# Performance work log

Hardware: AMD Instinct MI355X
Metric: run time of the kernel (lower is better)

The kernel has to match this reference:

```python
import jax, jax.numpy as jnp
import numpy as np

B, N, IN_DIM, DIM, KNN = 8, 2048, 128, 128, 16
POS_H = 64
ATTN_H = DIM * 4
EPS = 1e-5
SCALE = 1.0 / np.sqrt(DIM).astype(np.float32)


def setup_inputs() -> dict:
    key = jax.random.key(0)
    ks = jax.random.split(key, 10)
    nrm = lambda k, shape, s=0.02: jax.random.normal(k, shape, jnp.float32) * s
    return dict(
        ori_x=jax.random.normal(ks[0], (B, N, IN_DIM), jnp.float32),
        pos=jax.random.normal(ks[1], (B, N, 3), jnp.float32),
        w_in=nrm(ks[2], (IN_DIM, DIM)),
        w_qkv=nrm(ks[3], (DIM, 3 * DIM)),
        w_out=nrm(ks[4], (DIM, IN_DIM)),
        pos_w1=nrm(ks[5], (3, POS_H)), pos_b1=jnp.zeros((POS_H,), jnp.float32),
        pos_bn_g=jnp.ones((POS_H,), jnp.float32), pos_bn_b=jnp.zeros((POS_H,), jnp.float32),
        pos_bn_m=jnp.zeros((POS_H,), jnp.float32), pos_bn_v=jnp.ones((POS_H,), jnp.float32),
        pos_w2=nrm(ks[6], (POS_H, DIM)), pos_b2=jnp.zeros((DIM,), jnp.float32),
        attn_w1=nrm(ks[7], (DIM, ATTN_H)), attn_b1=jnp.zeros((ATTN_H,), jnp.float32),
        attn_bn_g=jnp.ones((ATTN_H,), jnp.float32), attn_bn_b=jnp.zeros((ATTN_H,), jnp.float32),
        attn_bn_m=jnp.zeros((ATTN_H,), jnp.float32), attn_bn_v=jnp.ones((ATTN_H,), jnp.float32),
        attn_w2=nrm(ks[8], (ATTN_H, DIM)), attn_b2=jnp.zeros((DIM,), jnp.float32),
    )


def _bn_eval(x, g, b, m, v):
    # BatchNorm2d in eval mode; channel is the last axis in our [b,n,k,C] layout
    return (x - m) * (g * jax.lax.rsqrt(v + EPS)) + b


def reference(ori_x, pos, w_in, w_qkv, w_out,
              pos_w1, pos_b1, pos_bn_g, pos_bn_b, pos_bn_m, pos_bn_v, pos_w2, pos_b2,
              attn_w1, attn_b1, attn_bn_g, attn_bn_b, attn_bn_m, attn_bn_v, attn_w2, attn_b2):
    x = ori_x @ w_in                                  # [b,n,dim]
    qkv = x @ w_qkv
    q, k, v = jnp.split(qkv, 3, axis=-1)              # each [b,n,dim]

    # pairwise squared distances [b,n,n] (monotone in rel_dist -> same topk)
    sq = jnp.sum(pos * pos, axis=-1)
    d2 = sq[:, :, None] + sq[:, None, :] - 2.0 * jnp.einsum('bnd,bmd->bnm', pos, pos)
    _, idx = jax.lax.top_k(-d2, KNN)                  # [b,n,KNN] nearest neighbors

    gather = jax.vmap(lambda t, i: t[i])              # [n,C],[n,k] -> [n,k,C] per batch
    k_g = gather(k, idx)                              # [b,n,k,dim]
    v_g = gather(v, idx)
    pos_g = gather(pos, idx)                          # [b,n,k,3]

    rel_pos = pos[:, :, None, :] - pos_g              # [b,n,k,3]
    pe = jax.nn.relu(_bn_eval(rel_pos @ pos_w1 + pos_b1, pos_bn_g, pos_bn_b, pos_bn_m, pos_bn_v))
    pe = pe @ pos_w2 + pos_b2                         # [b,n,k,dim]

    qk_rel = q[:, :, None, :] - k_g                   # [b,n,k,dim]
    h = jax.nn.relu(_bn_eval((qk_rel + pe) @ attn_w1 + attn_b1,
                             attn_bn_g, attn_bn_b, attn_bn_m, attn_bn_v))
    h = h @ attn_w2 + attn_b2                         # [b,n,k,dim]

    attn = jax.nn.softmax(h * SCALE, axis=-2)         # softmax over neighbors
    agg = jnp.sum(attn * (v_g + pe), axis=2)          # [b,n,dim]
    return agg @ w_out + ori_x
```

## Files before the change

kernel.cpp:

```cpp
#include <hip/hip_runtime.h>

#define EPS 1e-5f

constexpr int NB   = 8;
constexpr int NN   = 2048;
constexpr int DIM  = 128;
constexpr int KNN  = 16;
constexpr int AH   = 512;
constexpr int NPTS = NB * NN;
constexpr float SCALE = 0.08838834764831845f;

typedef __attribute__((ext_vector_type(8))) short short8;
typedef __attribute__((ext_vector_type(4))) float floatx4;

__device__ __forceinline__ short f2bf(float f) {
  union { float f; unsigned u; } a; a.f = f;
  return (short)((a.u + 0x8000u) >> 16);
}
__device__ __forceinline__ float bf2f(short s) {
  union { unsigned u; float f; } a; a.u = ((unsigned)(unsigned short)s) << 16;
  return a.f;
}

__global__ __launch_bounds__(256) void pack_weights(
    const float* __restrict__ attn_w1, const float* __restrict__ attn_w2,
    const float* __restrict__ pos_w2, const float* __restrict__ w_in,
    const float* __restrict__ w_qkv,
    const float* __restrict__ w_out, const float* __restrict__ pos,
    const float* __restrict__ attn_b1, const float* __restrict__ abn_g,
    const float* __restrict__ abn_b, const float* __restrict__ abn_m,
    const float* __restrict__ abn_v,
    const float* __restrict__ pos_b1, const float* __restrict__ pbn_g,
    const float* __restrict__ pbn_b, const float* __restrict__ pbn_m,
    const float* __restrict__ pbn_v, const float* __restrict__ pos_b2,
    short* __restrict__ w1p, short* __restrict__ w2p, short* __restrict__ pw2p,
    short* __restrict__ wfp, short* __restrict__ wop,
    float* __restrict__ biasq,
    float* __restrict__ t1sc, float* __restrict__ t1bi,
    float* __restrict__ phsc, float* __restrict__ phbi,
    float* __restrict__ pos_t)
{
  int t = blockIdx.x * 256 + threadIdx.x;
  if (t < 65536) {
    int k = t >> 9, n = t & 511;
    int ks = k >> 5, q = (k >> 3) & 3, j = k & 7;
    int ch = n >> 6, nt = (n >> 4) & 3, cc = n & 15;
    int dst = ch * 8192 + nt * 2048 + ks * 512 + (q * 16 + cc) * 8 + j;
    w1p[dst] = f2bf(attn_w1[t]);
  } else if (t < 131072) {
    int s = t - 65536;
    int k = s >> 7, n = s & 127;
    int ch = k >> 6, r = k & 63;
    int ks = r >> 5, q = (r >> 3) & 3, j = r & 7;
    int nt = n >> 4, cc = n & 15;
    int dst = ch * 8192 + nt * 1024 + ks * 512 + (q * 16 + cc) * 8 + j;
    w2p[dst] = f2bf(attn_w2[s]);
  } else if (t < 139264) {
    int s = t - 131072;
    int k = s >> 7, n = s & 127;
    int ks = k >> 5, r = k & 31, q = r >> 3, j = r & 7;
    int nt = n >> 4, cc = n & 15;
    int dst = nt * 1024 + ks * 512 + (q * 16 + cc) * 8 + j;
    pw2p[dst] = f2bf(pos_w2[s]);
  } else if (t < 188416) {
    int e = t - 139264;
    int j = e & 7, lane = (e >> 3) & 63, ks = (e >> 9) & 3, nt = (e >> 11) & 7, nc = e >> 14;
    int q = lane >> 4, cc = lane & 15;
    int k = ks * 32 + q * 8 + j, n = nc * 128 + nt * 16 + cc;
    float s = 0.0f;
#pragma unroll 8
    for (int m = 0; m < 128; ++m)
      s += w_in[(size_t)k * DIM + m] * w_qkv[(size_t)m * 384 + n];
    wfp[e] = f2bf(s);
  } else if (t < 204800) {
    int s = t - 188416;
    int k = s >> 7, n = s & 127;
    int ks = k >> 5, q = (k >> 3) & 3, j = k & 7;
    int nt = n >> 4, cc = n & 15;
    int dst = nt * 2048 + ks * 512 + (q * 16 + cc) * 8 + j;
    wop[dst] = f2bf(w_out[s]);
  } else if (t < 205184) {
    int c = t - 204800;
    biasq[c] = (c < 128) ? pos_b2[c] : ((c < 256) ? 0.0f : pos_b2[c - 256]);
  } else if (t < 205696) {
    int c = t - 205184;
    t1sc[c] = abn_g[c] * rsqrtf(abn_v[c] + EPS);
  } else if (t < 206208) {
    int c = t - 205696;
    float sc = abn_g[c] * rsqrtf(abn_v[c] + EPS);
    t1bi[c] = (attn_b1[c] - abn_m[c]) * sc + abn_b[c];
  } else if (t < 206272) {
    int c = t - 206208;
    phsc[c] = pbn_g[c] * rsqrtf(pbn_v[c] + EPS);
  } else if (t < 206336) {
    int c = t - 206272;
    float sc = pbn_g[c] * rsqrtf(pbn_v[c] + EPS);
    phbi[c] = (pos_b1[c] - pbn_m[c]) * sc + pbn_b[c];
  } else if (t < 206336 + NPTS * 3) {
    int e = t - 206336;
    int p = e / 3, d = e - p * 3;
    int b = p >> 11, n = p & (NN - 1);
    pos_t[((size_t)b * 3 + d) * NN + n] = pos[e];
  }
}

__global__ __launch_bounds__(256, 4) void knn_gemm_in(
    const float* __restrict__ A, const short* __restrict__ wfp,
    const float* __restrict__ biasq, short* __restrict__ C,
    const float* __restrict__ pos_t, int* __restrict__ idx_out)
{
  __shared__ short As[64 * 128];
  const int tid = threadIdx.x;
  const int bx = blockIdx.x;

  if (bx % 9 == 0) {
    const int lane = tid & 63, w = tid >> 6;
    const int wr = w >> 1, wc = w & 1;
    const int q = lane >> 4, cc = lane & 15;
    const int row0 = (bx / 9) * 64;
#pragma unroll
    for (int it = 0; it < 4; ++it) {
      int e = tid + it * 256;
      int row = e >> 4, cg = e & 15;
      const float* src = A + (size_t)(row0 + row) * 128 + cg * 8;
      float4 f0 = *(const float4*)src, f1 = *(const float4*)(src + 4);
      short8 v;
      v[0] = f2bf(f0.x); v[1] = f2bf(f0.y); v[2] = f2bf(f0.z); v[3] = f2bf(f0.w);
      v[4] = f2bf(f1.x); v[5] = f2bf(f1.y); v[6] = f2bf(f1.z); v[7] = f2bf(f1.w);
      *(short8*)(As + row * 128 + ((cg ^ (row & 15)) << 3)) = v;
    }
    __syncthreads();
    for (int nc = 0; nc < 3; ++nc) {
      floatx4 acc[2][4];
#pragma unroll
      for (int i = 0; i < 2; ++i)
#pragma unroll
        for (int jt = 0; jt < 4; ++jt) acc[i][jt] = (floatx4){0.f, 0.f, 0.f, 0.f};
#pragma unroll
      for (int ks = 0; ks < 4; ++ks) {
        short8 a8[2], b8[4];
#pragma unroll
        for (int i = 0; i < 2; ++i) {
          int row = (wr * 2 + i) * 16 + cc;
          a8[i] = *(const short8*)(As + row * 128 + (((ks * 4 + q) ^ cc) << 3));
        }
#pragma unroll
        for (int jt = 0; jt < 4; ++jt)
          b8[jt] = *(const short8*)(wfp + ((((nc * 8 + wc * 4 + jt) * 4 + ks) * 64 + lane) << 3));
#pragma unroll
        for (int i = 0; i < 2; ++i)
#pragma unroll
          for (int jt = 0; jt < 4; ++jt)
            acc[i][jt] = __builtin_amdgcn_mfma_f32_16x16x32_bf16(a8[i], b8[jt], acc[i][jt], 0, 0, 0);
      }
#pragma unroll
      for (int jt = 0; jt < 4; ++jt) {
        int colG = nc * 128 + (wc * 4 + jt) * 16 + cc;
        float bv = biasq[colG];
#pragma unroll
        for (int i = 0; i < 2; ++i)
#pragma unroll
          for (int r = 0; r < 4; ++r) {
            int row = (wr * 2 + i) * 16 + q * 4 + r;
            C[(size_t)(row0 + row) * 384 + colG] = f2bf(acc[i][jt][r] + bv);
          }
      }
    }
  } else {
    const int kb = bx - bx / 9 - 1;
    const int lane = tid & 63;
    const int p0 = kb * 8 + (tid >> 6) * 2;
    const int b = p0 >> 11, i0 = p0 & (NN - 1), i1 = i0 + 1;
    const float* px = pos_t + (size_t)b * 3 * NN;
    const float* py = px + NN;
    const float* pz = py + NN;
    const float xa = px[i0], ya = py[i0], za = pz[i0];
    const float sqa = xa * xa + ya * ya + za * za;
    const float xb = px[i1], yb = py[i1], zb = pz[i1];
    const float sqb = xb * xb + yb * yb + zb * zb;
    float va[32], vb[32];
#pragma unroll
    for (int t = 0; t < 32; ++t) {
      int j = t * 64 + lane;
      float xj = px[j], yj = py[j], zj = pz[j];
      float sqj = xj * xj + yj * yj + zj * zj;
      va[t] = sqa + sqj - 2.0f * (xa * xj + ya * yj + za * zj);
      vb[t] = sqb + sqj - 2.0f * (xb * xj + yb * yj + zb * zj);
    }
    for (int s = 0; s < KNN; ++s) {
      float av = 3.4e38f; int aj = 1 << 30;
      float bv = 3.4e38f; int bj = 1 << 30;
#pragma unroll
      for (int t = 0; t < 32; ++t) {
        if (va[t] < av) { av = va[t]; aj = t * 64 + lane; }
        if (vb[t] < bv) { bv = vb[t]; bj = t * 64 + lane; }
      }
#pragma unroll
      for (int m = 1; m < 64; m <<= 1) {
        float oav = __shfl_xor(av, m); int oaj = __shfl_xor(aj, m);
        float obv = __shfl_xor(bv, m); int obj = __shfl_xor(bj, m);
        if (oav < av || (oav == av && oaj < aj)) { av = oav; aj = oaj; }
        if (obv < bv || (obv == bv && obj < bj)) { bv = obv; bj = obj; }
      }
      if (lane == 0) {
        idx_out[(size_t)p0 * KNN + s] = aj;
        idx_out[(size_t)(p0 + 1) * KNN + s] = bj;
      }
#pragma unroll
      for (int t = 0; t < 32; ++t) {
        if (aj == t * 64 + lane) va[t] = 3.4e38f;
        if (bj == t * 64 + lane) vb[t] = 3.4e38f;
      }
    }
  }
}

__global__ __launch_bounds__(256, 3) void fused_attn(
    const float* __restrict__ pos_t, const short* __restrict__ qkv,
    const int* __restrict__ knn_idx,
    const float* __restrict__ pos_w1,
    const short* __restrict__ w1p, const short* __restrict__ w2p,
    const short* __restrict__ pw2p, const short* __restrict__ wop,
    const float* __restrict__ t1sc, const float* __restrict__ t1bi,
    const float* __restrict__ phsc, const float* __restrict__ phbi,
    const float* __restrict__ attn_b2,
    const float* __restrict__ ori_x, float* __restrict__ out)
{
  __shared__ short a_s[64 * 128];
  __shared__ short vpe_s[64 * 128];
  __shared__ short t1_s[2][64 * 64];
  __shared__ short q_ss[4 * 128];
  __shared__ float relp_s[64 * 4];
  __shared__ int   nbr_s[64];

  const int tid = threadIdx.x;
  const int lane = tid & 63, w = tid >> 6;
  const int wr = w >> 1, wc = w & 1;
  const int q = lane >> 4, cc = lane & 15;
  const int bb = blockIdx.x & 7;
  const int base = (blockIdx.x >> 3) * 4;
  const int gp0 = bb * NN + base;

  const float* px = pos_t + (size_t)bb * 3 * NN;
  const float* py = px + NN;
  const float* pz = py + NN;

  if (tid < 64) nbr_s[tid] = knn_idx[(size_t)gp0 * KNN + tid];
  else if (tid < 128) {
    int e = tid - 64;
    int p = e >> 4, seg = e & 15;
    *(short8*)(q_ss + p * 128 + seg * 8) =
        *(const short8*)(qkv + (size_t)(gp0 + p) * 384 + seg * 8);
  }
  __syncthreads();
  if (tid < 64) {
    int p = tid >> 4;
    int j = nbr_s[tid];
    relp_s[tid * 4 + 0] = px[base + p] - px[j];
    relp_s[tid * 4 + 1] = py[base + p] - py[j];
    relp_s[tid * 4 + 2] = pz[base + p] - pz[j];
  }
  __syncthreads();

#pragma unroll
  for (int r2 = 0; r2 < 16; ++r2) {
    int e = tid + r2 * 256;
    int row = e >> 6, c = e & 63;
    float lin = relp_s[row * 4] * pos_w1[c] + relp_s[row * 4 + 1] * pos_w1[64 + c]
              + relp_s[row * 4 + 2] * pos_w1[128 + c];
    t1_s[0][row * 64 + (((c >> 3) ^ (row & 7)) << 3) + (c & 7)] =
        f2bf(fmaxf(lin * phsc[c] + phbi[c], 0.0f));
  }
  __syncthreads();

  floatx4 pe[2][4];
#pragma unroll
  for (int i = 0; i < 2; ++i)
#pragma unroll
    for (int jt = 0; jt < 4; ++jt) pe[i][jt] = (floatx4){0.f, 0.f, 0.f, 0.f};
#pragma unroll
  for (int ks = 0; ks < 2; ++ks) {
    short8 a8[2];
#pragma unroll
    for (int i = 0; i < 2; ++i) {
      int row = (wr * 2 + i) * 16 + cc;
      a8[i] = *(const short8*)(t1_s[0] + row * 64 + (((ks * 4 + q) ^ (row & 7)) << 3));
    }
#pragma unroll
    for (int jt = 0; jt < 4; ++jt) {
      short8 b8 = *(const short8*)(pw2p + ((((wc * 4 + jt) * 2 + ks) * 64 + lane) << 3));
#pragma unroll
      for (int i = 0; i < 2; ++i)
        pe[i][jt] = __builtin_amdgcn_mfma_f32_16x16x32_bf16(a8[i], b8, pe[i][jt], 0, 0, 0);
    }
  }

#pragma unroll
  for (int it = 0; it < 4; ++it) {
    int e = tid + it * 256;
    int row = e >> 4, g = e & 15;
    const short* kvrow = qkv + ((size_t)bb * NN + nbr_s[row]) * 384;
    int dst = row * 128 + ((g ^ (row & 15)) << 3);
    *(short8*)(a_s + dst)   = *(const short8*)(kvrow + 128 + g * 8);
    *(short8*)(vpe_s + dst) = *(const short8*)(kvrow + 256 + g * 8);
  }
  __syncthreads();

#pragma unroll
  for (int i = 0; i < 2; ++i) {
    int rt = wr * 2 + i;
#pragma unroll
    for (int jt = 0; jt < 4; ++jt) {
      int col = (wc * 4 + jt) * 16 + cc;
      float qv = bf2f(q_ss[rt * 128 + col]);
#pragma unroll
      for (int r = 0; r < 4; ++r) {
        int row = rt * 16 + q * 4 + r;
        float pev = pe[i][jt][r];
        int slot = row * 128 + (((col >> 3) ^ (row & 15)) << 3) + (col & 7);
        a_s[slot]   = f2bf(qv - bf2f(a_s[slot]) + pev);
        vpe_s[slot] = f2bf(bf2f(vpe_s[slot]) + pev);
      }
    }
  }
  __syncthreads();

  floatx4 hacc[2][4];
#pragma unroll
  for (int i = 0; i < 2; ++i)
#pragma unroll
    for (int jt = 0; jt < 4; ++jt) hacc[i][jt] = (floatx4){0.f, 0.f, 0.f, 0.f};

  for (int ch = 0; ch < 8; ++ch) {
    short* t1b = t1_s[ch & 1];
    floatx4 tacc[2][2];
#pragma unroll
    for (int i = 0; i < 2; ++i)
#pragma unroll
      for (int jt = 0; jt < 2; ++jt) tacc[i][jt] = (floatx4){0.f, 0.f, 0.f, 0.f};
#pragma unroll
    for (int ks = 0; ks < 4; ++ks) {
      short8 a8[2], b8[2];
#pragma unroll
      for (int i = 0; i < 2; ++i) {
        int row = (wr * 2 + i) * 16 + cc;
        a8[i] = *(const short8*)(a_s + row * 128 + (((ks * 4 + q) ^ cc) << 3));
      }
#pragma unroll
      for (int jt = 0; jt < 2; ++jt)
        b8[jt] = *(const short8*)(w1p + ((((ch * 4 + wc * 2 + jt) * 4 + ks) * 64 + lane) << 3));
#pragma unroll
      for (int i = 0; i < 2; ++i)
#pragma unroll
        for (int jt = 0; jt < 2; ++jt)
          tacc[i][jt] = __builtin_amdgcn_mfma_f32_16x16x32_bf16(a8[i], b8[jt], tacc[i][jt], 0, 0, 0);
    }
#pragma unroll
    for (int jt = 0; jt < 2; ++jt) {
      int colL = (wc * 2 + jt) * 16 + cc;
      int colG = ch * 64 + colL;
      float sc = t1sc[colG], bi = t1bi[colG];
#pragma unroll
      for (int i = 0; i < 2; ++i)
#pragma unroll
        for (int r = 0; r < 4; ++r) {
          int row = (wr * 2 + i) * 16 + q * 4 + r;
          t1b[row * 64 + (((colL >> 3) ^ (row & 7)) << 3) + (colL & 7)] =
              f2bf(fmaxf(tacc[i][jt][r] * sc + bi, 0.0f));
        }
    }
    __syncthreads();
#pragma unroll
    for (int ks = 0; ks < 2; ++ks) {
      short8 a8[2], b8[4];
#pragma unroll
      for (int i = 0; i < 2; ++i) {
        int row = (wr * 2 + i) * 16 + cc;
        a8[i] = *(const short8*)(t1b + row * 64 + (((ks * 4 + q) ^ (row & 7)) << 3));
      }
#pragma unroll
      for (int jt = 0; jt < 4; ++jt)
        b8[jt] = *(const short8*)(w2p + ((((ch * 8 + wc * 4 + jt) * 2 + ks) * 64 + lane) << 3));
#pragma unroll
      for (int i = 0; i < 2; ++i)
#pragma unroll
        for (int jt = 0; jt < 4; ++jt)
          hacc[i][jt] = __builtin_amdgcn_mfma_f32_16x16x32_bf16(a8[i], b8[jt], hacc[i][jt], 0, 0, 0);
    }
  }

  short* agg_s = t1_s[0];
#pragma unroll
  for (int i = 0; i < 2; ++i) {
    int rt = wr * 2 + i;
#pragma unroll
    for (int jt = 0; jt < 4; ++jt) {
      int col = (wc * 4 + jt) * 16 + cc;
      float b2v = attn_b2[col];
      float v0[4], mx = -3.4e38f;
#pragma unroll
      for (int r = 0; r < 4; ++r) {
        v0[r] = (hacc[i][jt][r] + b2v) * SCALE;
        mx = fmaxf(mx, v0[r]);
      }
      mx = fmaxf(mx, __shfl_xor(mx, 16));
      mx = fmaxf(mx, __shfl_xor(mx, 32));
      float ex[4], sum = 0.f;
#pragma unroll
      for (int r = 0; r < 4; ++r) { ex[r] = __expf(v0[r] - mx); sum += ex[r]; }
      sum += __shfl_xor(sum, 16);
      sum += __shfl_xor(sum, 32);
      float inv = 1.0f / sum;
      float part = 0.f;
#pragma unroll
      for (int r = 0; r < 4; ++r) {
        int row = rt * 16 + q * 4 + r;
        int slot = row * 128 + (((col >> 3) ^ (row & 15)) << 3) + (col & 7);
        part += ex[r] * bf2f(vpe_s[slot]);
      }
      part += __shfl_xor(part, 16);
      part += __shfl_xor(part, 32);
      if (q == 0) agg_s[rt * 136 + col] = f2bf(part * inv);
    }
  }
  __syncthreads();

  {
    floatx4 oacc[2];
#pragma unroll
    for (int jt = 0; jt < 2; ++jt) oacc[jt] = (floatx4){0.f, 0.f, 0.f, 0.f};
#pragma unroll
    for (int ks = 0; ks < 4; ++ks) {
      short8 a8 = *(const short8*)(agg_s + cc * 136 + ks * 32 + q * 8);
#pragma unroll
      for (int jt = 0; jt < 2; ++jt) {
        short8 b8 = *(const short8*)(wop + ((((w * 2 + jt) * 4 + ks) * 64 + lane) << 3));
        oacc[jt] = __builtin_amdgcn_mfma_f32_16x16x32_bf16(a8, b8, oacc[jt], 0, 0, 0);
      }
    }
    if (q == 0) {
#pragma unroll
      for (int jt = 0; jt < 2; ++jt) {
        int col = (w * 2 + jt) * 16 + cc;
#pragma unroll
        for (int r = 0; r < 4; ++r) {
          size_t o = (size_t)(gp0 + r) * 128 + col;
          out[o] = oacc[jt][r] + ori_x[o];
        }
      }
    }
  }
}

extern "C" void kernel_launch(void* const* d_in, const int* in_sizes, int n_in,
                              void* d_out, int out_size, void* d_ws, size_t ws_size,
                              hipStream_t stream)
{
  const float* ori_x    = (const float*)d_in[0];
  const float* pos      = (const float*)d_in[1];
  const float* w_in     = (const float*)d_in[2];
  const float* w_qkv    = (const float*)d_in[3];
  const float* w_out    = (const float*)d_in[4];
  const float* pos_w1   = (const float*)d_in[5];
  const float* pos_b1   = (const float*)d_in[6];
  const float* pos_bn_g = (const float*)d_in[7];
  const float* pos_bn_b = (const float*)d_in[8];
  const float* pos_bn_m = (const float*)d_in[9];
  const float* pos_bn_v = (const float*)d_in[10];
  const float* pos_w2   = (const float*)d_in[11];
  const float* pos_b2   = (const float*)d_in[12];
  const float* attn_w1  = (const float*)d_in[13];
  const float* attn_b1  = (const float*)d_in[14];
  const float* attn_bn_g = (const float*)d_in[15];
  const float* attn_bn_b = (const float*)d_in[16];
  const float* attn_bn_m = (const float*)d_in[17];
  const float* attn_bn_v = (const float*)d_in[18];
  const float* attn_w2  = (const float*)d_in[19];
  const float* attn_b2  = (const float*)d_in[20];
  float* out = (float*)d_out;

  short* qkvb = (short*)d_ws;
  short* w1p  = qkvb + (size_t)NPTS * 3 * DIM;
  short* w2p  = w1p + 65536;
  short* pw2p = w2p + 65536;
  short* wfp  = pw2p + 8192;
  short* wop  = wfp + 49152;
  float* biasq = (float*)(wop + 16384);
  float* t1sc = biasq + 384;
  float* t1bi = t1sc + 512;
  float* phsc = t1bi + 512;
  float* phbi = phsc + 64;
  float* pos_t = phbi + 64;
  int*   idx  = (int*)(pos_t + (size_t)NB * 3 * NN);

  pack_weights<<<998, 256, 0, stream>>>(attn_w1, attn_w2, pos_w2, w_in, w_qkv,
      w_out, pos,
      attn_b1, attn_bn_g, attn_bn_b, attn_bn_m, attn_bn_v,
      pos_b1, pos_bn_g, pos_bn_b, pos_bn_m, pos_bn_v, pos_b2,
      w1p, w2p, pw2p, wfp, wop, biasq, t1sc, t1bi, phsc, phbi, pos_t);
  knn_gemm_in<<<2304, 256, 0, stream>>>(ori_x, wfp, biasq, qkvb, pos_t, idx);
  fused_attn<<<NPTS / 4, 256, 0, stream>>>(pos_t, qkvb, idx, pos_w1,
      w1p, w2p, pw2p, wop, t1sc, t1bi, phsc, phbi, attn_b2, ori_x, out);
}
```

Before: 361.9 us.

## Fold BN scales into weights and shrink fused_attn LDS for higher occupancy

Folds the batch-norm scale factors of both MLPs into the packed first-layer weights (attn_w1 and pos_w1), so the epilogues only add a bias. fused_attn's shared memory is cut by dropping the double-buffered t1 tile, the q/neighbor/relpos staging buffers and two of the three prologue barriers. Neighbor indices and q values are now read straight from global memory, and launch bounds are raised to 4 blocks per SM. The single t1 buffer needs an extra barrier in every chunk iteration, and the higher occupancy target may push registers to spill.

```diff
diff --git a/kernel.cpp b/kernel.cpp
--- a/kernel.cpp
+++ b/kernel.cpp
@@ -27,6 +27,7 @@
     const float* __restrict__ pos_w2, const float* __restrict__ w_in,
     const float* __restrict__ w_qkv,
     const float* __restrict__ w_out, const float* __restrict__ pos,
+    const float* __restrict__ pos_w1,
     const float* __restrict__ attn_b1, const float* __restrict__ abn_g,
     const float* __restrict__ abn_b, const float* __restrict__ abn_m,
     const float* __restrict__ abn_v,
@@ -35,9 +36,8 @@
     const float* __restrict__ pbn_v, const float* __restrict__ pos_b2,
     short* __restrict__ w1p, short* __restrict__ w2p, short* __restrict__ pw2p,
     short* __restrict__ wfp, short* __restrict__ wop,
-    float* __restrict__ biasq,
-    float* __restrict__ t1sc, float* __restrict__ t1bi,
-    float* __restrict__ phsc, float* __restrict__ phbi,
+    float* __restrict__ biasq, float* __restrict__ t1bi,
+    float* __restrict__ phbi, float* __restrict__ w1s,
     float* __restrict__ pos_t)
 {
   int t = blockIdx.x * 256 + threadIdx.x;
@@ -46,7 +46,8 @@
     int ks = k >> 5, q = (k >> 3) & 3, j = k & 7;
     int ch = n >> 6, nt = (n >> 4) & 3, cc = n & 15;
     int dst = ch * 8192 + nt * 2048 + ks * 512 + (q * 16 + cc) * 8 + j;
-    w1p[dst] = f2bf(attn_w1[t]);
+    float sc = abn_g[n] * rsqrtf(abn_v[n] + EPS);
+    w1p[dst] = f2bf(attn_w1[t] * sc);
   } else if (t < 131072) {
     int s = t - 65536;
     int k = s >> 7, n = s & 127;
@@ -84,20 +85,19 @@
     biasq[c] = (c < 128) ? pos_b2[c] : ((c < 256) ? 0.0f : pos_b2[c - 256]);
   } else if (t < 205696) {
     int c = t - 205184;
-    t1sc[c] = abn_g[c] * rsqrtf(abn_v[c] + EPS);
-  } else if (t < 206208) {
-    int c = t - 205696;
     float sc = abn_g[c] * rsqrtf(abn_v[c] + EPS);
     t1bi[c] = (attn_b1[c] - abn_m[c]) * sc + abn_b[c];
-  } else if (t < 206272) {
-    int c = t - 206208;
-    phsc[c] = pbn_g[c] * rsqrtf(pbn_v[c] + EPS);
-  } else if (t < 206336) {
-    int c = t - 206272;
+  } else if (t < 205760) {
+    int c = t - 205696;
     float sc = pbn_g[c] * rsqrtf(pbn_v[c] + EPS);
     phbi[c] = (pos_b1[c] - pbn_m[c]) * sc + pbn_b[c];
-  } else if (t < 206336 + NPTS * 3) {
-    int e = t - 206336;
+  } else if (t < 205952) {
+    int e = t - 205760;
+    int c = e & 63;
+    float sc = pbn_g[c] * rsqrtf(pbn_v[c] + EPS);
+    w1s[e] = pos_w1[e] * sc;
+  } else if (t < 205952 + NPTS * 3) {
+    int e = t - 205952;
     int p = e / 3, d = e - p * 3;
     int b = p >> 11, n = p & (NN - 1);
     pos_t[((size_t)b * 3 + d) * NN + n] = pos[e];
@@ -215,23 +215,19 @@
   }
 }
 
-__global__ __launch_bounds__(256, 3) void fused_attn(
+__global__ __launch_bounds__(256, 4) void fused_attn(
     const float* __restrict__ pos_t, const short* __restrict__ qkv,
     const int* __restrict__ knn_idx,
-    const float* __restrict__ pos_w1,
+    const float* __restrict__ w1s,
     const short* __restrict__ w1p, const short* __restrict__ w2p,
     const short* __restrict__ pw2p, const short* __restrict__ wop,
-    const float* __restrict__ t1sc, const float* __restrict__ t1bi,
-    const float* __restrict__ phsc, const float* __restrict__ phbi,
+    const float* __restrict__ t1bi, const float* __restrict__ phbi,
     const float* __restrict__ attn_b2,
     const float* __restrict__ ori_x, float* __restrict__ out)
 {
   __shared__ short a_s[64 * 128];
   __shared__ short vpe_s[64 * 128];
-  __shared__ short t1_s[2][64 * 64];
-  __shared__ short q_ss[4 * 128];
-  __shared__ float relp_s[64 * 4];
-  __shared__ int   nbr_s[64];
+  __shared__ short t1_s[64 * 64];
 
   const int tid = threadIdx.x;
   const int lane = tid & 63, w = tid >> 6;
@@ -245,74 +241,65 @@
   const float* py = px + NN;
   const float* pz = py + NN;
 
-  if (tid < 64) nbr_s[tid] = knn_idx[(size_t)gp0 * KNN + tid];
-  else if (tid < 128) {
-    int e = tid - 64;
-    int p = e >> 4, seg = e & 15;
-    *(short8*)(q_ss + p * 128 + seg * 8) =
-        *(const short8*)(qkv + (size_t)(gp0 + p) * 384 + seg * 8);
-  }
-  __syncthreads();
-  if (tid < 64) {
-    int p = tid >> 4;
-    int j = nbr_s[tid];
-    relp_s[tid * 4 + 0] = px[base + p] - px[j];
-    relp_s[tid * 4 + 1] = py[base + p] - py[j];
-    relp_s[tid * 4 + 2] = pz[base + p] - pz[j];
-  }
-  __syncthreads();
-
-#pragma unroll
-  for (int r2 = 0; r2 < 16; ++r2) {
-    int e = tid + r2 * 256;
-    int row = e >> 6, c = e & 63;
-    float lin = relp_s[row * 4] * pos_w1[c] + relp_s[row * 4 + 1] * pos_w1[64 + c]
-              + relp_s[row * 4 + 2] * pos_w1[128 + c];
-    t1_s[0][row * 64 + (((c >> 3) ^ (row & 7)) << 3) + (c & 7)] =
-        f2bf(fmaxf(lin * phsc[c] + phbi[c], 0.0f));
-  }
-  __syncthreads();
-
-  floatx4 pe[2][4];
-#pragma unroll
-  for (int i = 0; i < 2; ++i)
-#pragma unroll
-    for (int jt = 0; jt < 4; ++jt) pe[i][jt] = (floatx4){0.f, 0.f, 0.f, 0.f};
-#pragma unroll
-  for (int ks = 0; ks < 2; ++ks) {
-    short8 a8[2];
-#pragma unroll
-    for (int i = 0; i < 2; ++i) {
-      int row = (wr * 2 + i) * 16 + cc;
-      a8[i] = *(const short8*)(t1_s[0] + row * 64 + (((ks * 4 + q) ^ (row & 7)) << 3));
-    }
-#pragma unroll
-    for (int jt = 0; jt < 4; ++jt) {
-      short8 b8 = *(const short8*)(pw2p + ((((wc * 4 + jt) * 2 + ks) * 64 + lane) << 3));
-#pragma unroll
-      for (int i = 0; i < 2; ++i)
-        pe[i][jt] = __builtin_amdgcn_mfma_f32_16x16x32_bf16(a8[i], b8, pe[i][jt], 0, 0, 0);
-    }
-  }
-
+  {
+    int row = tid >> 2, q4 = (tid & 3) * 16;
+    int p = row >> 4;
+    int j = knn_idx[(size_t)gp0 * KNN + row];
+    float rx = px[base + p] - px[j];
+    float ry = py[base + p] - py[j];
+    float rz = pz[base + p] - pz[j];
+#pragma unroll
+    for (int u = 0; u < 16; ++u) {
+      int c = q4 + u;
+      float lin = rx * w1s[c] + ry * w1s[64 + c] + rz * w1s[128 + c] + phbi[c];
+      t1_s[row * 64 + (((c >> 3) ^ (row & 7)) << 3) + (c & 7)] =
+          f2bf(fmaxf(lin, 0.0f));
+    }
+  }
+  int nbrr[4];
+#pragma unroll
+  for (int it = 0; it < 4; ++it)
+    nbrr[it] = knn_idx[(size_t)gp0 * KNN + (tid >> 4) + it * 16];
 #pragma unroll
   for (int it = 0; it < 4; ++it) {
     int e = tid + it * 256;
     int row = e >> 4, g = e & 15;
-    const short* kvrow = qkv + ((size_t)bb * NN + nbr_s[row]) * 384;
+    const short* kvrow = qkv + ((size_t)bb * NN + nbrr[it]) * 384;
     int dst = row * 128 + ((g ^ (row & 15)) << 3);
     *(short8*)(a_s + dst)   = *(const short8*)(kvrow + 128 + g * 8);
     *(short8*)(vpe_s + dst) = *(const short8*)(kvrow + 256 + g * 8);
   }
   __syncthreads();
 
+  floatx4 pe[2][4];
+#pragma unroll
+  for (int i = 0; i < 2; ++i)
+#pragma unroll
+    for (int jt = 0; jt < 4; ++jt) pe[i][jt] = (floatx4){0.f, 0.f, 0.f, 0.f};
+#pragma unroll
+  for (int ks = 0; ks < 2; ++ks) {
+    short8 a8[2];
+#pragma unroll
+    for (int i = 0; i < 2; ++i) {
+      int row = (wr * 2 + i) * 16 + cc;
+      a8[i] = *(const short8*)(t1_s + row * 64 + (((ks * 4 + q) ^ (row & 7)) << 3));
+    }
+#pragma unroll
+    for (int jt = 0; jt < 4; ++jt) {
+      short8 b8 = *(const short8*)(pw2p + ((((wc * 4 + jt) * 2 + ks) * 64 + lane) << 3));
+#pragma unroll
+      for (int i = 0; i < 2; ++i)
+        pe[i][jt] = __builtin_amdgcn_mfma_f32_16x16x32_bf16(a8[i], b8, pe[i][jt], 0, 0, 0);
+    }
+  }
+
 #pragma unroll
   for (int i = 0; i < 2; ++i) {
     int rt = wr * 2 + i;
 #pragma unroll
     for (int jt = 0; jt < 4; ++jt) {
       int col = (wc * 4 + jt) * 16 + cc;
-      float qv = bf2f(q_ss[rt * 128 + col]);
+      float qv = bf2f(qkv[(size_t)(gp0 + rt) * 384 + col]);
 #pragma unroll
       for (int r = 0; r < 4; ++r) {
         int row = rt * 16 + q * 4 + r;
@@ -332,7 +319,6 @@
     for (int jt = 0; jt < 4; ++jt) hacc[i][jt] = (floatx4){0.f, 0.f, 0.f, 0.f};
 
   for (int ch = 0; ch < 8; ++ch) {
-    short* t1b = t1_s[ch & 1];
     floatx4 tacc[2][2];
 #pragma unroll
     for (int i = 0; i < 2; ++i)
@@ -355,18 +341,18 @@
         for (int jt = 0; jt < 2; ++jt)
           tacc[i][jt] = __builtin_amdgcn_mfma_f32_16x16x32_bf16(a8[i], b8[jt], tacc[i][jt], 0, 0, 0);
     }
+    __syncthreads();
 #pragma unroll
     for (int jt = 0; jt < 2; ++jt) {
       int colL = (wc * 2 + jt) * 16 + cc;
-      int colG = ch * 64 + colL;
-      float sc = t1sc[colG], bi = t1bi[colG];
+      float bi = t1bi[ch * 64 + colL];
 #pragma unroll
       for (int i = 0; i < 2; ++i)
 #pragma unroll
         for (int r = 0; r < 4; ++r) {
           int row = (wr * 2 + i) * 16 + q * 4 + r;
-          t1b[row * 64 + (((colL >> 3) ^ (row & 7)) << 3) + (colL & 7)] =
-              f2bf(fmaxf(tacc[i][jt][r] * sc + bi, 0.0f));
+          t1_s[row * 64 + (((colL >> 3) ^ (row & 7)) << 3) + (colL & 7)] =
+              f2bf(fmaxf(tacc[i][jt][r] + bi, 0.0f));
         }
     }
     __syncthreads();
@@ -376,7 +362,7 @@
 #pragma unroll
       for (int i = 0; i < 2; ++i) {
         int row = (wr * 2 + i) * 16 + cc;
-        a8[i] = *(const short8*)(t1b + row * 64 + (((ks * 4 + q) ^ (row & 7)) << 3));
+        a8[i] = *(const short8*)(t1_s + row * 64 + (((ks * 4 + q) ^ (row & 7)) << 3));
       }
 #pragma unroll
       for (int jt = 0; jt < 4; ++jt)
@@ -388,8 +374,9 @@
           hacc[i][jt] = __builtin_amdgcn_mfma_f32_16x16x32_bf16(a8[i], b8[jt], hacc[i][jt], 0, 0, 0);
     }
   }
-
-  short* agg_s = t1_s[0];
+  __syncthreads();
+
+  short* agg_s = t1_s;
 #pragma unroll
   for (int i = 0; i < 2; ++i) {
     int rt = wr * 2 + i;
@@ -486,19 +473,18 @@
   short* wfp  = pw2p + 8192;
   short* wop  = wfp + 49152;
   float* biasq = (float*)(wop + 16384);
-  float* t1sc = biasq + 384;
-  float* t1bi = t1sc + 512;
-  float* phsc = t1bi + 512;
-  float* phbi = phsc + 64;
-  float* pos_t = phbi + 64;
+  float* t1bi = biasq + 384;
+  float* phbi = t1bi + 512;
+  float* w1s  = phbi + 64;
+  float* pos_t = w1s + 192;
   int*   idx  = (int*)(pos_t + (size_t)NB * 3 * NN);
 
-  pack_weights<<<998, 256, 0, stream>>>(attn_w1, attn_w2, pos_w2, w_in, w_qkv,
-      w_out, pos,
+  pack_weights<<<997, 256, 0, stream>>>(attn_w1, attn_w2, pos_w2, w_in, w_qkv,
+      w_out, pos, pos_w1,
       attn_b1, attn_bn_g, attn_bn_b, attn_bn_m, attn_bn_v,
       pos_b1, pos_bn_g, pos_bn_b, pos_bn_m, pos_bn_v, pos_b2,
-      w1p, w2p, pw2p, wfp, wop, biasq, t1sc, t1bi, phsc, phbi, pos_t);
+      w1p, w2p, pw2p, wfp, wop, biasq, t1bi, phbi, w1s, pos_t);
   knn_gemm_in<<<2304, 256, 0, stream>>>(ori_x, wfp, biasq, qkvb, pos_t, idx);
-  fused_attn<<<NPTS / 4, 256, 0, stream>>>(pos_t, qkvb, idx, pos_w1,
-      w1p, w2p, pw2p, wop, t1sc, t1bi, phsc, phbi, attn_b2, ori_x, out);
-}
+  fused_attn<<<NPTS / 4, 256, 0, stream>>>(pos_t, qkvb, idx, w1s,
+      w1p, w2p, pw2p, wop, t1bi, phbi, attn_b2, ori_x, out);
+}
```

Result: slower. 373.5 us (+3.2%).
